# Performance work log

Measured on AMD Instinct MI355X. Metric: run time of the kernel, lower is better.

## Reference

```python
import jax, jax.numpy as jnp
import numpy as np

B, L, D = 32, 128, 128


def setup_inputs() -> dict:
    key = jax.random.key(0)
    ks = jax.random.split(key, 10)
    s = 1.0 / np.sqrt(D)  # torch nn.Linear default init bound
    inp = {
        "input_real": jax.random.normal(ks[0], (B, L, D), jnp.float32),
        "input_imag": jax.random.normal(ks[1], (B, L, D), jnp.float32),
        "Wr1": jax.random.uniform(ks[2], (D, D), jnp.float32, -s, s),
        "br1": jax.random.uniform(ks[3], (D,), jnp.float32, -s, s),
        "Wi1": jax.random.uniform(ks[4], (D, D), jnp.float32, -s, s),
        "bi1": jax.random.uniform(ks[5], (D,), jnp.float32, -s, s),
        "Wr2": jax.random.uniform(ks[6], (D, D), jnp.float32, -s, s),
        "br2": jax.random.uniform(ks[7], (D,), jnp.float32, -s, s),
        "Wi2": jax.random.uniform(ks[8], (D, D), jnp.float32, -s, s),
        "bi2": jax.random.uniform(ks[9], (D,), jnp.float32, -s, s),
    }
    return inp


def reference(input_real, input_imag, Wr1, br1, Wi1, bi1, Wr2, br2, Wi2, bi2):
    # torch Linear: y = x @ W.T + b
    r1 = input_real @ Wr1.T + br1            # (B, L, D)
    i1 = input_imag @ Wi1.T + bi1
    diag_real1 = r1 * r1 - i1 * i1           # Re((r1+i*i1)^2)
    diag_imag1 = 2.0 * r1 * i1               # Im((r1+i*i1)^2)

    r2 = input_real @ Wr2.T + br2
    i2 = input_imag @ Wi2.T + bi2
    diag_real2 = r2 * r2 - i2 * i2
    diag_imag2 = 2.0 * r2 * i2

    # attention over sequence positions L
    att_real = jax.nn.softmax(jnp.sum(diag_real1 * diag_real2, axis=-1), axis=-1)  # (B, L)
    att_imag = jax.nn.softmax(jnp.sum(diag_imag1 * diag_imag2, axis=-1), axis=-1)  # (B, L)

    # Weighted sum over L of per-token complex outer products, without
    # materializing the (B, L, D, D) intermediates the torch code builds:
    # Matrix_real[l] = r2 r2^T - i2 i2^T ; Matrix_imag[l] = i2 r2^T + r2 i2^T
    Mr = (jnp.einsum('bl,bld,ble->bde', att_real, r2, r2)
          - jnp.einsum('bl,bld,ble->bde', att_real, i2, i2))   # (B, D, D)
    Mi = (jnp.einsum('bl,bld,ble->bde', att_imag, i2, r2)
          + jnp.einsum('bl,bld,ble->bde', att_imag, r2, i2))   # (B, D, D)
    return (Mr, Mi)
```

## Files before the change

### kernel.cpp

```cpp
#include <hip/hip_runtime.h>
#include <hip/hip_bf16.h>
#include <math.h>

#define NB 32
#define NL 128
#define ND 128

typedef __attribute__((ext_vector_type(8))) short bf16x8;
typedef __attribute__((ext_vector_type(4))) float f32x4;

union F4  { float4 v; float f[4]; };
union BF8 { bf16x8 v; ushort u[8]; };

__device__ inline ushort f2bf(float f) {
    __hip_bfloat16 h = __float2bfloat16(f);
    union { __hip_bfloat16 h; ushort u; } c; c.h = h; return c.u;
}
__device__ inline float bf2f(ushort u) {
    union { unsigned int i; float f; } c; c.i = ((unsigned int)u) << 16; return c.f;
}
__device__ inline short2 bsplit(float f) {
    ushort hu = f2bf(f);
    short2 r;
    r.x = (short)hu;
    r.y = (short)f2bf(f - bf2f(hu));
    return r;
}

__global__ __launch_bounds__(256) void k_proj(
    const float* __restrict__ xr, const float* __restrict__ xi,
    const float* __restrict__ Wr1, const float* __restrict__ br1,
    const float* __restrict__ Wi1, const float* __restrict__ bi1,
    const float* __restrict__ Wr2, const float* __restrict__ br2,
    const float* __restrict__ Wi2, const float* __restrict__ bi2,
    ushort* __restrict__ gtb, float* __restrict__ lgG)
{
    __shared__ float lgpart[2 * 4 * 16];

    const int bid   = blockIdx.x;
    const int t     = threadIdx.x;
    const int w     = t >> 6;
    const int lane  = t & 63;
    const int l15   = lane & 15;
    const int koff8 = (lane >> 4) * 8;
    const int b     = bid >> 3;
    const int lt    = bid & 7;
    const int arowg = b * NL + lt * 16 + l15;

    bf16x8 axh[2][4], axl[2][4];
    {
        const float* xs[2] = {xr, xi};
#pragma unroll
        for (int arr = 0; arr < 2; ++arr)
#pragma unroll
            for (int ks = 0; ks < 4; ++ks) {
                const float* p = xs[arr] + (size_t)arowg * ND + ks * 32 + koff8;
                F4 f0, f1;
                f0.v = *(const float4*)&p[0];
                f1.v = *(const float4*)&p[4];
                bf16x8 h, l;
#pragma unroll
                for (int e = 0; e < 4; ++e) {
                    short2 s = bsplit(f0.f[e]); h[e] = s.x; l[e] = s.y;
                }
#pragma unroll
                for (int e = 0; e < 4; ++e) {
                    short2 s = bsplit(f1.f[e]); h[4 + e] = s.x; l[4 + e] = s.y;
                }
                axh[arr][ks] = h;
                axl[arr][ks] = l;
            }
    }

    f32x4 acc[4][2];
#pragma unroll
    for (int m = 0; m < 4; ++m)
#pragma unroll
        for (int n = 0; n < 2; ++n) acc[m][n] = (f32x4){0.f, 0.f, 0.f, 0.f};

    {
        const float* Ws[4] = {Wr1, Wi1, Wr2, Wi2};
#pragma unroll
        for (int mat = 0; mat < 4; ++mat) {
            const int arr = mat & 1;
#pragma unroll
            for (int n = 0; n < 2; ++n) {
                const float* wrow = Ws[mat] + (size_t)((w * 2 + n) * 16 + l15) * ND;
#pragma unroll
                for (int ks = 0; ks < 4; ++ks) {
                    F4 f0, f1;
                    f0.v = *(const float4*)&wrow[ks * 32 + koff8];
                    f1.v = *(const float4*)&wrow[ks * 32 + koff8 + 4];
                    bf16x8 bh, bl;
#pragma unroll
                    for (int e = 0; e < 4; ++e) {
                        short2 s = bsplit(f0.f[e]); bh[e] = s.x; bl[e] = s.y;
                    }
#pragma unroll
                    for (int e = 0; e < 4; ++e) {
                        short2 s = bsplit(f1.f[e]); bh[4 + e] = s.x; bl[4 + e] = s.y;
                    }
                    acc[mat][n] = __builtin_amdgcn_mfma_f32_16x16x32_bf16(axh[arr][ks], bh, acc[mat][n], 0, 0, 0);
                    acc[mat][n] = __builtin_amdgcn_mfma_f32_16x16x32_bf16(axh[arr][ks], bl, acc[mat][n], 0, 0, 0);
                    acc[mat][n] = __builtin_amdgcn_mfma_f32_16x16x32_bf16(axl[arr][ks], bh, acc[mat][n], 0, 0, 0);
                }
            }
        }
    }

    float pR[4] = {0.f, 0.f, 0.f, 0.f};
    float pI[4] = {0.f, 0.f, 0.f, 0.f};
    const int lbase = lt * 16 + (lane >> 4) * 4;
#pragma unroll
    for (int n = 0; n < 2; ++n) {
        const int d = (w * 2 + n) * 16 + l15;
        const float b0 = br1[d], b1 = bi1[d], b2 = br2[d], b3 = bi2[d];
        ushort g2[4], g3[4];
#pragma unroll
        for (int r = 0; r < 4; ++r) {
            float y0 = acc[0][n][r] + b0;
            float y1 = acc[1][n][r] + b1;
            float y2 = acc[2][n][r] + b2;
            float y3 = acc[3][n][r] + b3;
            pR[r] += (y0 * y0 - y1 * y1) * (y2 * y2 - y3 * y3);
            pI[r] += 4.f * y0 * y1 * y2 * y3;
            g2[r] = f2bf(y2);
            g3[r] = f2bf(y3);
        }
        ushort4 q2 = {g2[0], g2[1], g2[2], g2[3]};
        ushort4 q3 = {g3[0], g3[1], g3[2], g3[3]};
        *(ushort4*)&gtb[((size_t)(0 * NB + b) * ND + d) * NL + lbase] = q2;
        *(ushort4*)&gtb[((size_t)(1 * NB + b) * ND + d) * NL + lbase] = q3;
    }

#pragma unroll
    for (int off = 1; off < 16; off <<= 1)
#pragma unroll
        for (int r = 0; r < 4; ++r) {
            pR[r] += __shfl_xor(pR[r], off);
            pI[r] += __shfl_xor(pI[r], off);
        }
    if (l15 == 0) {
        const int row = (lane >> 4) * 4;
#pragma unroll
        for (int r = 0; r < 4; ++r) {
            lgpart[(0 * 4 + w) * 16 + row + r] = pR[r];
            lgpart[(1 * 4 + w) * 16 + row + r] = pI[r];
        }
    }
    __syncthreads();
    if (t < 32) {
        const int c = t >> 4, row = t & 15;
        float s = lgpart[(c * 4 + 0) * 16 + row] + lgpart[(c * 4 + 1) * 16 + row]
                + lgpart[(c * 4 + 2) * 16 + row] + lgpart[(c * 4 + 3) * 16 + row];
        lgG[(size_t)(c * NB + b) * NL + lt * 16 + row] = s;
    }
}

__global__ __launch_bounds__(256) void k_gram(
    const ushort* __restrict__ gtb, const float* __restrict__ lgG,
    float* __restrict__ out)
{
    extern __shared__ char L[];
    float* wfl  = (float*)(L + 65536);
    float* wred = (float*)(L + 66048);

    const int bid   = blockIdx.x;
    const int t     = threadIdx.x;
    const int w     = t >> 6;
    const int lane  = t & 63;
    const int l15   = lane & 15;
    const int koff8 = (lane >> 4) * 8;
    const int koffb = koff8 * 2;

    const int b    = bid >> 3;
    const int sub  = bid & 7;
    const int term = sub >> 2;
    const int dq   = (sub >> 1) & 1;
    const int eo   = sub & 1;

    float sv = 0.f, se = 0.f;
    if (t < 128) {
        sv = lgG[(size_t)(term * NB + b) * NL + t];
        float m = sv;
#pragma unroll
        for (int off = 1; off < 64; off <<= 1) m = fmaxf(m, __shfl_xor(m, off));
        if (lane == 0) wred[w] = m;
    }
    __syncthreads();
    if (t < 128) {
        float m = fmaxf(wred[0], wred[1]);
        se = expf(sv - m);
        float s = se;
#pragma unroll
        for (int off = 1; off < 64; off <<= 1) s += __shfl_xor(s, off);
        if (lane == 0) wred[2 + w] = s;
    }
    __syncthreads();
    if (t < 128) wfl[t] = se / (wred[2] + wred[3]);

#pragma unroll
    for (int j = 0; j < 16; ++j) {
        int u    = t + 256 * j;
        int arr  = u >> 11;
        int row  = (u >> 4) & 127;
        int slot = u & 15;
        bf16x8 v = *(const bf16x8*)&gtb[((size_t)(arr * NB + b) * ND + row) * NL + slot * 8];
        *(bf16x8*)(L + arr * 32768 + row * 256 + ((slot * 16) ^ ((row & 7) << 4))) = v;
    }
    __syncthreads();

    f32x4 accP[4], accN[4];
#pragma unroll
    for (int nt = 0; nt < 4; ++nt) {
        accP[nt] = (f32x4){0.f, 0.f, 0.f, 0.f};
        accN[nt] = (f32x4){0.f, 0.f, 0.f, 0.f};
    }

#pragma unroll
    for (int ks = 0; ks < 4; ++ks) {
        F4 w0, w1;
        w0.v = *(const float4*)&wfl[ks * 32 + koff8];
        w1.v = *(const float4*)&wfl[ks * 32 + koff8 + 4];
        float wv[8] = {w0.f[0], w0.f[1], w0.f[2], w0.f[3],
                       w1.f[0], w1.f[1], w1.f[2], w1.f[3]};

        const int ar = dq * 64 + w * 16 + l15;
        const int ab = ar * 256 + (((ks * 64) + koffb) ^ ((ar & 7) << 4));
        BF8 a0; a0.v = *(const bf16x8*)(L + ab);
        BF8 a1; a1.v = *(const bf16x8*)(L + 32768 + ab);
        bf16x8 s0, s1;
#pragma unroll
        for (int e = 0; e < 8; ++e) {
            s0[e] = (short)f2bf(bf2f(a0.u[e]) * wv[e]);
            s1[e] = (short)f2bf(bf2f(a1.u[e]) * wv[e]);
        }
        bf16x8 aP = term ? s1 : s0;
        bf16x8 aN = term ? s0 : s1;

#pragma unroll
        for (int nt = 0; nt < 4; ++nt) {
            const int br = eo * 64 + nt * 16 + l15;
            const int bb = br * 256 + (((ks * 64) + koffb) ^ ((br & 7) << 4));
            bf16x8 b0 = *(const bf16x8*)(L + bb);
            bf16x8 b1 = *(const bf16x8*)(L + 32768 + bb);
            accP[nt] = __builtin_amdgcn_mfma_f32_16x16x32_bf16(aP, b0, accP[nt], 0, 0, 0);
            accN[nt] = __builtin_amdgcn_mfma_f32_16x16x32_bf16(aN, b1, accN[nt], 0, 0, 0);
        }
    }

    const float sgn = term ? 1.f : -1.f;
    float* dst = out + (size_t)term * NB * ND * ND + (size_t)b * ND * ND;
    const int rb = dq * 64 + w * 16 + (lane >> 4) * 4;
#pragma unroll
    for (int nt = 0; nt < 4; ++nt) {
        const int ec = eo * 64 + nt * 16 + l15;
#pragma unroll
        for (int r = 0; r < 4; ++r)
            dst[(size_t)(rb + r) * ND + ec] = accP[nt][r] + sgn * accN[nt][r];
    }
}

extern "C" void kernel_launch(void* const* d_in, const int* in_sizes, int n_in,
                              void* d_out, int out_size, void* d_ws, size_t ws_size,
                              hipStream_t stream)
{
    const float* xr  = (const float*)d_in[0];
    const float* xi  = (const float*)d_in[1];
    const float* Wr1 = (const float*)d_in[2];
    const float* br1 = (const float*)d_in[3];
    const float* Wi1 = (const float*)d_in[4];
    const float* bi1 = (const float*)d_in[5];
    const float* Wr2 = (const float*)d_in[6];
    const float* br2 = (const float*)d_in[7];
    const float* Wi2 = (const float*)d_in[8];
    const float* bi2 = (const float*)d_in[9];

    ushort* gtb = (ushort*)d_ws;
    float*  lgG = (float*)(gtb + 2 * NB * ND * NL);

    (void)hipFuncSetAttribute((const void*)k_gram,
                              hipFuncAttributeMaxDynamicSharedMemorySize, 66560);

    hipLaunchKernelGGL(k_proj, dim3(256), dim3(256), 0, stream,
                       xr, xi, Wr1, br1, Wi1, bi1, Wr2, br2, Wi2, bi2,
                       gtb, lgG);
    hipLaunchKernelGGL(k_gram, dim3(256), dim3(256), 66560, stream,
                       gtb, lgG, (float*)d_out);
}
```

Measured before the change: 25.25 us.

## Fuse projection and gram kernels into one launch with per-batch atomic counters

Merges the two kernels into a single 512-block launch. The first 256 blocks compute the projections and bump a per-batch counter after a threadfence, and the remaining blocks spin on that counter before doing softmax and the gram MFMAs. This removes the kernel-to-kernel launch gap and lets gram work for early batches overlap projection for later ones. It adds a memset launch, spin-wait overhead, and a deadlock risk if consumer blocks take all the slots before producers are scheduled. The projection blocks also now request 66 KB of dynamic LDS, which may lower their occupancy.

```diff
diff --git a/kernel.cpp b/kernel.cpp
--- a/kernel.cpp
+++ b/kernel.cpp
@@ -27,143 +27,16 @@
     return r;
 }
 
-__global__ __launch_bounds__(256) void k_proj(
+__global__ __launch_bounds__(256) void k_all(
     const float* __restrict__ xr, const float* __restrict__ xi,
     const float* __restrict__ Wr1, const float* __restrict__ br1,
     const float* __restrict__ Wi1, const float* __restrict__ bi1,
     const float* __restrict__ Wr2, const float* __restrict__ br2,
     const float* __restrict__ Wi2, const float* __restrict__ bi2,
-    ushort* __restrict__ gtb, float* __restrict__ lgG)
-{
-    __shared__ float lgpart[2 * 4 * 16];
-
-    const int bid   = blockIdx.x;
-    const int t     = threadIdx.x;
-    const int w     = t >> 6;
-    const int lane  = t & 63;
-    const int l15   = lane & 15;
-    const int koff8 = (lane >> 4) * 8;
-    const int b     = bid >> 3;
-    const int lt    = bid & 7;
-    const int arowg = b * NL + lt * 16 + l15;
-
-    bf16x8 axh[2][4], axl[2][4];
-    {
-        const float* xs[2] = {xr, xi};
-#pragma unroll
-        for (int arr = 0; arr < 2; ++arr)
-#pragma unroll
-            for (int ks = 0; ks < 4; ++ks) {
-                const float* p = xs[arr] + (size_t)arowg * ND + ks * 32 + koff8;
-                F4 f0, f1;
-                f0.v = *(const float4*)&p[0];
-                f1.v = *(const float4*)&p[4];
-                bf16x8 h, l;
-#pragma unroll
-                for (int e = 0; e < 4; ++e) {
-                    short2 s = bsplit(f0.f[e]); h[e] = s.x; l[e] = s.y;
-                }
-#pragma unroll
-                for (int e = 0; e < 4; ++e) {
-                    short2 s = bsplit(f1.f[e]); h[4 + e] = s.x; l[4 + e] = s.y;
-                }
-                axh[arr][ks] = h;
-                axl[arr][ks] = l;
-            }
-    }
-
-    f32x4 acc[4][2];
-#pragma unroll
-    for (int m = 0; m < 4; ++m)
-#pragma unroll
-        for (int n = 0; n < 2; ++n) acc[m][n] = (f32x4){0.f, 0.f, 0.f, 0.f};
-
-    {
-        const float* Ws[4] = {Wr1, Wi1, Wr2, Wi2};
-#pragma unroll
-        for (int mat = 0; mat < 4; ++mat) {
-            const int arr = mat & 1;
-#pragma unroll
-            for (int n = 0; n < 2; ++n) {
-                const float* wrow = Ws[mat] + (size_t)((w * 2 + n) * 16 + l15) * ND;
-#pragma unroll
-                for (int ks = 0; ks < 4; ++ks) {
-                    F4 f0, f1;
-                    f0.v = *(const float4*)&wrow[ks * 32 + koff8];
-                    f1.v = *(const float4*)&wrow[ks * 32 + koff8 + 4];
-                    bf16x8 bh, bl;
-#pragma unroll
-                    for (int e = 0; e < 4; ++e) {
-                        short2 s = bsplit(f0.f[e]); bh[e] = s.x; bl[e] = s.y;
-                    }
-#pragma unroll
-                    for (int e = 0; e < 4; ++e) {
-                        short2 s = bsplit(f1.f[e]); bh[4 + e] = s.x; bl[4 + e] = s.y;
-                    }
-                    acc[mat][n] = __builtin_amdgcn_mfma_f32_16x16x32_bf16(axh[arr][ks], bh, acc[mat][n], 0, 0, 0);
-                    acc[mat][n] = __builtin_amdgcn_mfma_f32_16x16x32_bf16(axh[arr][ks], bl, acc[mat][n], 0, 0, 0);
-                    acc[mat][n] = __builtin_amdgcn_mfma_f32_16x16x32_bf16(axl[arr][ks], bh, acc[mat][n], 0, 0, 0);
-                }
-            }
-        }
-    }
-
-    float pR[4] = {0.f, 0.f, 0.f, 0.f};
-    float pI[4] = {0.f, 0.f, 0.f, 0.f};
-    const int lbase = lt * 16 + (lane >> 4) * 4;
-#pragma unroll
-    for (int n = 0; n < 2; ++n) {
-        const int d = (w * 2 + n) * 16 + l15;
-        const float b0 = br1[d], b1 = bi1[d], b2 = br2[d], b3 = bi2[d];
-        ushort g2[4], g3[4];
-#pragma unroll
-        for (int r = 0; r < 4; ++r) {
-            float y0 = acc[0][n][r] + b0;
-            float y1 = acc[1][n][r] + b1;
-            float y2 = acc[2][n][r] + b2;
-            float y3 = acc[3][n][r] + b3;
-            pR[r] += (y0 * y0 - y1 * y1) * (y2 * y2 - y3 * y3);
-            pI[r] += 4.f * y0 * y1 * y2 * y3;
-            g2[r] = f2bf(y2);
-            g3[r] = f2bf(y3);
-        }
-        ushort4 q2 = {g2[0], g2[1], g2[2], g2[3]};
-        ushort4 q3 = {g3[0], g3[1], g3[2], g3[3]};
-        *(ushort4*)&gtb[((size_t)(0 * NB + b) * ND + d) * NL + lbase] = q2;
-        *(ushort4*)&gtb[((size_t)(1 * NB + b) * ND + d) * NL + lbase] = q3;
-    }
-
-#pragma unroll
-    for (int off = 1; off < 16; off <<= 1)
-#pragma unroll
-        for (int r = 0; r < 4; ++r) {
-            pR[r] += __shfl_xor(pR[r], off);
-            pI[r] += __shfl_xor(pI[r], off);
-        }
-    if (l15 == 0) {
-        const int row = (lane >> 4) * 4;
-#pragma unroll
-        for (int r = 0; r < 4; ++r) {
-            lgpart[(0 * 4 + w) * 16 + row + r] = pR[r];
-            lgpart[(1 * 4 + w) * 16 + row + r] = pI[r];
-        }
-    }
-    __syncthreads();
-    if (t < 32) {
-        const int c = t >> 4, row = t & 15;
-        float s = lgpart[(c * 4 + 0) * 16 + row] + lgpart[(c * 4 + 1) * 16 + row]
-                + lgpart[(c * 4 + 2) * 16 + row] + lgpart[(c * 4 + 3) * 16 + row];
-        lgG[(size_t)(c * NB + b) * NL + lt * 16 + row] = s;
-    }
-}
-
-__global__ __launch_bounds__(256) void k_gram(
-    const ushort* __restrict__ gtb, const float* __restrict__ lgG,
+    int* __restrict__ cnt, ushort* __restrict__ gtb, float* __restrict__ lgG,
     float* __restrict__ out)
 {
     extern __shared__ char L[];
-    float* wfl  = (float*)(L + 65536);
-    float* wred = (float*)(L + 66048);
 
     const int bid   = blockIdx.x;
     const int t     = threadIdx.x;
@@ -173,91 +46,224 @@
     const int koff8 = (lane >> 4) * 8;
     const int koffb = koff8 * 2;
 
-    const int b    = bid >> 3;
-    const int sub  = bid & 7;
-    const int term = sub >> 2;
-    const int dq   = (sub >> 1) & 1;
-    const int eo   = sub & 1;
-
-    float sv = 0.f, se = 0.f;
-    if (t < 128) {
-        sv = lgG[(size_t)(term * NB + b) * NL + t];
-        float m = sv;
-#pragma unroll
-        for (int off = 1; off < 64; off <<= 1) m = fmaxf(m, __shfl_xor(m, off));
-        if (lane == 0) wred[w] = m;
-    }
-    __syncthreads();
-    if (t < 128) {
-        float m = fmaxf(wred[0], wred[1]);
-        se = expf(sv - m);
-        float s = se;
-#pragma unroll
-        for (int off = 1; off < 64; off <<= 1) s += __shfl_xor(s, off);
-        if (lane == 0) wred[2 + w] = s;
-    }
-    __syncthreads();
-    if (t < 128) wfl[t] = se / (wred[2] + wred[3]);
-
-#pragma unroll
-    for (int j = 0; j < 16; ++j) {
-        int u    = t + 256 * j;
-        int arr  = u >> 11;
-        int row  = (u >> 4) & 127;
-        int slot = u & 15;
-        bf16x8 v = *(const bf16x8*)&gtb[((size_t)(arr * NB + b) * ND + row) * NL + slot * 8];
-        *(bf16x8*)(L + arr * 32768 + row * 256 + ((slot * 16) ^ ((row & 7) << 4))) = v;
-    }
-    __syncthreads();
-
-    f32x4 accP[4], accN[4];
-#pragma unroll
-    for (int nt = 0; nt < 4; ++nt) {
-        accP[nt] = (f32x4){0.f, 0.f, 0.f, 0.f};
-        accN[nt] = (f32x4){0.f, 0.f, 0.f, 0.f};
-    }
-
-#pragma unroll
-    for (int ks = 0; ks < 4; ++ks) {
-        F4 w0, w1;
-        w0.v = *(const float4*)&wfl[ks * 32 + koff8];
-        w1.v = *(const float4*)&wfl[ks * 32 + koff8 + 4];
-        float wv[8] = {w0.f[0], w0.f[1], w0.f[2], w0.f[3],
-                       w1.f[0], w1.f[1], w1.f[2], w1.f[3]};
-
-        const int ar = dq * 64 + w * 16 + l15;
-        const int ab = ar * 256 + (((ks * 64) + koffb) ^ ((ar & 7) << 4));
-        BF8 a0; a0.v = *(const bf16x8*)(L + ab);
-        BF8 a1; a1.v = *(const bf16x8*)(L + 32768 + ab);
-        bf16x8 s0, s1;
-#pragma unroll
-        for (int e = 0; e < 8; ++e) {
-            s0[e] = (short)f2bf(bf2f(a0.u[e]) * wv[e]);
-            s1[e] = (short)f2bf(bf2f(a1.u[e]) * wv[e]);
-        }
-        bf16x8 aP = term ? s1 : s0;
-        bf16x8 aN = term ? s0 : s1;
-
+    if (bid < 256) {
+        float* lgpart = (float*)L;
+        const int b     = bid >> 3;
+        const int lt    = bid & 7;
+        const int arowg = b * NL + lt * 16 + l15;
+
+        bf16x8 axh[2][4], axl[2][4];
+        {
+            const float* xs[2] = {xr, xi};
+#pragma unroll
+            for (int arr = 0; arr < 2; ++arr)
+#pragma unroll
+                for (int ks = 0; ks < 4; ++ks) {
+                    const float* p = xs[arr] + (size_t)arowg * ND + ks * 32 + koff8;
+                    F4 f0, f1;
+                    f0.v = *(const float4*)&p[0];
+                    f1.v = *(const float4*)&p[4];
+                    bf16x8 h, l;
+#pragma unroll
+                    for (int e = 0; e < 4; ++e) {
+                        short2 s = bsplit(f0.f[e]); h[e] = s.x; l[e] = s.y;
+                    }
+#pragma unroll
+                    for (int e = 0; e < 4; ++e) {
+                        short2 s = bsplit(f1.f[e]); h[4 + e] = s.x; l[4 + e] = s.y;
+                    }
+                    axh[arr][ks] = h;
+                    axl[arr][ks] = l;
+                }
+        }
+
+        f32x4 acc[4][2];
+#pragma unroll
+        for (int m = 0; m < 4; ++m)
+#pragma unroll
+            for (int n = 0; n < 2; ++n) acc[m][n] = (f32x4){0.f, 0.f, 0.f, 0.f};
+
+        {
+            const float* Ws[4] = {Wr1, Wi1, Wr2, Wi2};
+#pragma unroll
+            for (int mat = 0; mat < 4; ++mat) {
+                const int arr = mat & 1;
+#pragma unroll
+                for (int n = 0; n < 2; ++n) {
+                    const float* wrow = Ws[mat] + (size_t)((w * 2 + n) * 16 + l15) * ND;
+#pragma unroll
+                    for (int ks = 0; ks < 4; ++ks) {
+                        F4 f0, f1;
+                        f0.v = *(const float4*)&wrow[ks * 32 + koff8];
+                        f1.v = *(const float4*)&wrow[ks * 32 + koff8 + 4];
+                        bf16x8 bh, bl;
+#pragma unroll
+                        for (int e = 0; e < 4; ++e) {
+                            short2 s = bsplit(f0.f[e]); bh[e] = s.x; bl[e] = s.y;
+                        }
+#pragma unroll
+                        for (int e = 0; e < 4; ++e) {
+                            short2 s = bsplit(f1.f[e]); bh[4 + e] = s.x; bl[4 + e] = s.y;
+                        }
+                        acc[mat][n] = __builtin_amdgcn_mfma_f32_16x16x32_bf16(axh[arr][ks], bh, acc[mat][n], 0, 0, 0);
+                        acc[mat][n] = __builtin_amdgcn_mfma_f32_16x16x32_bf16(axh[arr][ks], bl, acc[mat][n], 0, 0, 0);
+                        acc[mat][n] = __builtin_amdgcn_mfma_f32_16x16x32_bf16(axl[arr][ks], bh, acc[mat][n], 0, 0, 0);
+                    }
+                }
+            }
+        }
+
+        float pR[4] = {0.f, 0.f, 0.f, 0.f};
+        float pI[4] = {0.f, 0.f, 0.f, 0.f};
+        const int lbase = lt * 16 + (lane >> 4) * 4;
+#pragma unroll
+        for (int n = 0; n < 2; ++n) {
+            const int d = (w * 2 + n) * 16 + l15;
+            const float b0 = br1[d], b1 = bi1[d], b2 = br2[d], b3 = bi2[d];
+            ushort g2[4], g3[4];
+#pragma unroll
+            for (int r = 0; r < 4; ++r) {
+                float y0 = acc[0][n][r] + b0;
+                float y1 = acc[1][n][r] + b1;
+                float y2 = acc[2][n][r] + b2;
+                float y3 = acc[3][n][r] + b3;
+                pR[r] += (y0 * y0 - y1 * y1) * (y2 * y2 - y3 * y3);
+                pI[r] += 4.f * y0 * y1 * y2 * y3;
+                g2[r] = f2bf(y2);
+                g3[r] = f2bf(y3);
+            }
+            ushort4 q2 = {g2[0], g2[1], g2[2], g2[3]};
+            ushort4 q3 = {g3[0], g3[1], g3[2], g3[3]};
+            *(ushort4*)&gtb[((size_t)(0 * NB + b) * ND + d) * NL + lbase] = q2;
+            *(ushort4*)&gtb[((size_t)(1 * NB + b) * ND + d) * NL + lbase] = q3;
+        }
+
+#pragma unroll
+        for (int off = 1; off < 16; off <<= 1)
+#pragma unroll
+            for (int r = 0; r < 4; ++r) {
+                pR[r] += __shfl_xor(pR[r], off);
+                pI[r] += __shfl_xor(pI[r], off);
+            }
+        if (l15 == 0) {
+            const int row = (lane >> 4) * 4;
+#pragma unroll
+            for (int r = 0; r < 4; ++r) {
+                lgpart[(0 * 4 + w) * 16 + row + r] = pR[r];
+                lgpart[(1 * 4 + w) * 16 + row + r] = pI[r];
+            }
+        }
+        __syncthreads();
+        if (t < 32) {
+            const int c = t >> 4, row = t & 15;
+            float s = lgpart[(c * 4 + 0) * 16 + row] + lgpart[(c * 4 + 1) * 16 + row]
+                    + lgpart[(c * 4 + 2) * 16 + row] + lgpart[(c * 4 + 3) * 16 + row];
+            lgG[(size_t)(c * NB + b) * NL + lt * 16 + row] = s;
+        }
+
+        __threadfence();
+        __syncthreads();
+        if (t == 0) atomicAdd(&cnt[b * 16], 1);
+    } else {
+        float* wfl  = (float*)(L + 65536);
+        float* wred = (float*)(L + 66048);
+
+        const int gb   = bid - 256;
+        const int b    = gb >> 3;
+        const int sub  = gb & 7;
+        const int term = sub >> 2;
+        const int dq   = (sub >> 1) & 1;
+        const int eo   = sub & 1;
+
+        if (t == 0) {
+            while (__hip_atomic_load(&cnt[b * 16], __ATOMIC_ACQUIRE,
+                                     __HIP_MEMORY_SCOPE_AGENT) < 8) {
+                __builtin_amdgcn_s_sleep(8);
+            }
+        }
+        __syncthreads();
+        __threadfence();
+
+        float sv = 0.f, se = 0.f;
+        if (t < 128) {
+            sv = lgG[(size_t)(term * NB + b) * NL + t];
+            float m = sv;
+#pragma unroll
+            for (int off = 1; off < 64; off <<= 1) m = fmaxf(m, __shfl_xor(m, off));
+            if (lane == 0) wred[w] = m;
+        }
+        __syncthreads();
+        if (t < 128) {
+            float m = fmaxf(wred[0], wred[1]);
+            se = expf(sv - m);
+            float s = se;
+#pragma unroll
+            for (int off = 1; off < 64; off <<= 1) s += __shfl_xor(s, off);
+            if (lane == 0) wred[2 + w] = s;
+        }
+        __syncthreads();
+        if (t < 128) wfl[t] = se / (wred[2] + wred[3]);
+
+#pragma unroll
+        for (int j = 0; j < 16; ++j) {
+            int u    = t + 256 * j;
+            int arr  = u >> 11;
+            int row  = (u >> 4) & 127;
+            int slot = u & 15;
+            bf16x8 v = *(const bf16x8*)&gtb[((size_t)(arr * NB + b) * ND + row) * NL + slot * 8];
+            *(bf16x8*)(L + arr * 32768 + row * 256 + ((slot * 16) ^ ((row & 7) << 4))) = v;
+        }
+        __syncthreads();
+
+        f32x4 accP[4], accN[4];
 #pragma unroll
         for (int nt = 0; nt < 4; ++nt) {
-            const int br = eo * 64 + nt * 16 + l15;
-            const int bb = br * 256 + (((ks * 64) + koffb) ^ ((br & 7) << 4));
-            bf16x8 b0 = *(const bf16x8*)(L + bb);
-            bf16x8 b1 = *(const bf16x8*)(L + 32768 + bb);
-            accP[nt] = __builtin_amdgcn_mfma_f32_16x16x32_bf16(aP, b0, accP[nt], 0, 0, 0);
-            accN[nt] = __builtin_amdgcn_mfma_f32_16x16x32_bf16(aN, b1, accN[nt], 0, 0, 0);
-        }
-    }
-
-    const float sgn = term ? 1.f : -1.f;
-    float* dst = out + (size_t)term * NB * ND * ND + (size_t)b * ND * ND;
-    const int rb = dq * 64 + w * 16 + (lane >> 4) * 4;
-#pragma unroll
-    for (int nt = 0; nt < 4; ++nt) {
-        const int ec = eo * 64 + nt * 16 + l15;
-#pragma unroll
-        for (int r = 0; r < 4; ++r)
-            dst[(size_t)(rb + r) * ND + ec] = accP[nt][r] + sgn * accN[nt][r];
+            accP[nt] = (f32x4){0.f, 0.f, 0.f, 0.f};
+            accN[nt] = (f32x4){0.f, 0.f, 0.f, 0.f};
+        }
+
+#pragma unroll
+        for (int ks = 0; ks < 4; ++ks) {
+            F4 w0, w1;
+            w0.v = *(const float4*)&wfl[ks * 32 + koff8];
+            w1.v = *(const float4*)&wfl[ks * 32 + koff8 + 4];
+            float wv[8] = {w0.f[0], w0.f[1], w0.f[2], w0.f[3],
+                           w1.f[0], w1.f[1], w1.f[2], w1.f[3]};
+
+            const int ar = dq * 64 + w * 16 + l15;
+            const int ab = ar * 256 + (((ks * 64) + koffb) ^ ((ar & 7) << 4));
+            BF8 a0; a0.v = *(const bf16x8*)(L + ab);
+            BF8 a1; a1.v = *(const bf16x8*)(L + 32768 + ab);
+            bf16x8 s0, s1;
+#pragma unroll
+            for (int e = 0; e < 8; ++e) {
+                s0[e] = (short)f2bf(bf2f(a0.u[e]) * wv[e]);
+                s1[e] = (short)f2bf(bf2f(a1.u[e]) * wv[e]);
+            }
+            bf16x8 aP = term ? s1 : s0;
+            bf16x8 aN = term ? s0 : s1;
+
+#pragma unroll
+            for (int nt = 0; nt < 4; ++nt) {
+                const int br = eo * 64 + nt * 16 + l15;
+                const int bb = br * 256 + (((ks * 64) + koffb) ^ ((br & 7) << 4));
+                bf16x8 b0 = *(const bf16x8*)(L + bb);
+                bf16x8 b1 = *(const bf16x8*)(L + 32768 + bb);
+                accP[nt] = __builtin_amdgcn_mfma_f32_16x16x32_bf16(aP, b0, accP[nt], 0, 0, 0);
+                accN[nt] = __builtin_amdgcn_mfma_f32_16x16x32_bf16(aN, b1, accN[nt], 0, 0, 0);
+            }
+        }
+
+        const float sgn = term ? 1.f : -1.f;
+        float* dst = out + (size_t)term * NB * ND * ND + (size_t)b * ND * ND;
+        const int rb = dq * 64 + w * 16 + (lane >> 4) * 4;
+#pragma unroll
+        for (int nt = 0; nt < 4; ++nt) {
+            const int ec = eo * 64 + nt * 16 + l15;
+#pragma unroll
+            for (int r = 0; r < 4; ++r)
+                dst[(size_t)(rb + r) * ND + ec] = accP[nt][r] + sgn * accN[nt][r];
+        }
     }
 }
 
@@ -276,15 +282,15 @@
     const float* Wi2 = (const float*)d_in[8];
     const float* bi2 = (const float*)d_in[9];
 
-    ushort* gtb = (ushort*)d_ws;
+    int*    cnt = (int*)d_ws;
+    ushort* gtb = (ushort*)((char*)d_ws + 2048);
     float*  lgG = (float*)(gtb + 2 * NB * ND * NL);
 
-    (void)hipFuncSetAttribute((const void*)k_gram,
+    (void)hipFuncSetAttribute((const void*)k_all,
                               hipFuncAttributeMaxDynamicSharedMemorySize, 66560);
 
-    hipLaunchKernelGGL(k_proj, dim3(256), dim3(256), 0, stream,
+    hipMemsetAsync(cnt, 0, 2048, stream);
+    hipLaunchKernelGGL(k_all, dim3(512), dim3(256), 66560, stream,
                        xr, xi, Wr1, br1, Wi1, bi1, Wr2, br2, Wi2, bi2,
-                       gtb, lgG);
-    hipLaunchKernelGGL(k_gram, dim3(256), dim3(256), 66560, stream,
-                       gtb, lgG, (float*)d_out);
-}
+                       cnt, gtb, lgG, (float*)d_out);
+}
```

Result: slower. 98.93 us (+291.8%).

## Fuse projection and gram kernels, recomputing projections per block in LDS

Applied to the files above, without the earlier changes.

Merges the projection and gram kernels into one launch. Each block recomputes the full per-batch projections and writes the bf16 r2/i2 tiles directly into swizzled shared memory, and computes the attention logits locally. This removes the intermediate global buffer round trip and the second launch. The cost is 8x redundant projection MFMA and conversion work across the blocks of each batch.

```diff
diff --git a/kernel.cpp b/kernel.cpp
--- a/kernel.cpp
+++ b/kernel.cpp
@@ -27,145 +27,19 @@
     return r;
 }
 
-__global__ __launch_bounds__(256) void k_proj(
+__global__ __launch_bounds__(256, 1) void k_one(
     const float* __restrict__ xr, const float* __restrict__ xi,
     const float* __restrict__ Wr1, const float* __restrict__ br1,
     const float* __restrict__ Wi1, const float* __restrict__ bi1,
     const float* __restrict__ Wr2, const float* __restrict__ br2,
     const float* __restrict__ Wi2, const float* __restrict__ bi2,
-    ushort* __restrict__ gtb, float* __restrict__ lgG)
-{
-    __shared__ float lgpart[2 * 4 * 16];
-
-    const int bid   = blockIdx.x;
-    const int t     = threadIdx.x;
-    const int w     = t >> 6;
-    const int lane  = t & 63;
-    const int l15   = lane & 15;
-    const int koff8 = (lane >> 4) * 8;
-    const int b     = bid >> 3;
-    const int lt    = bid & 7;
-    const int arowg = b * NL + lt * 16 + l15;
-
-    bf16x8 axh[2][4], axl[2][4];
-    {
-        const float* xs[2] = {xr, xi};
-#pragma unroll
-        for (int arr = 0; arr < 2; ++arr)
-#pragma unroll
-            for (int ks = 0; ks < 4; ++ks) {
-                const float* p = xs[arr] + (size_t)arowg * ND + ks * 32 + koff8;
-                F4 f0, f1;
-                f0.v = *(const float4*)&p[0];
-                f1.v = *(const float4*)&p[4];
-                bf16x8 h, l;
-#pragma unroll
-                for (int e = 0; e < 4; ++e) {
-                    short2 s = bsplit(f0.f[e]); h[e] = s.x; l[e] = s.y;
-                }
-#pragma unroll
-                for (int e = 0; e < 4; ++e) {
-                    short2 s = bsplit(f1.f[e]); h[4 + e] = s.x; l[4 + e] = s.y;
-                }
-                axh[arr][ks] = h;
-                axl[arr][ks] = l;
-            }
-    }
-
-    f32x4 acc[4][2];
-#pragma unroll
-    for (int m = 0; m < 4; ++m)
-#pragma unroll
-        for (int n = 0; n < 2; ++n) acc[m][n] = (f32x4){0.f, 0.f, 0.f, 0.f};
-
-    {
-        const float* Ws[4] = {Wr1, Wi1, Wr2, Wi2};
-#pragma unroll
-        for (int mat = 0; mat < 4; ++mat) {
-            const int arr = mat & 1;
-#pragma unroll
-            for (int n = 0; n < 2; ++n) {
-                const float* wrow = Ws[mat] + (size_t)((w * 2 + n) * 16 + l15) * ND;
-#pragma unroll
-                for (int ks = 0; ks < 4; ++ks) {
-                    F4 f0, f1;
-                    f0.v = *(const float4*)&wrow[ks * 32 + koff8];
-                    f1.v = *(const float4*)&wrow[ks * 32 + koff8 + 4];
-                    bf16x8 bh, bl;
-#pragma unroll
-                    for (int e = 0; e < 4; ++e) {
-                        short2 s = bsplit(f0.f[e]); bh[e] = s.x; bl[e] = s.y;
-                    }
-#pragma unroll
-                    for (int e = 0; e < 4; ++e) {
-                        short2 s = bsplit(f1.f[e]); bh[4 + e] = s.x; bl[4 + e] = s.y;
-                    }
-                    acc[mat][n] = __builtin_amdgcn_mfma_f32_16x16x32_bf16(axh[arr][ks], bh, acc[mat][n], 0, 0, 0);
-                    acc[mat][n] = __builtin_amdgcn_mfma_f32_16x16x32_bf16(axh[arr][ks], bl, acc[mat][n], 0, 0, 0);
-                    acc[mat][n] = __builtin_amdgcn_mfma_f32_16x16x32_bf16(axl[arr][ks], bh, acc[mat][n], 0, 0, 0);
-                }
-            }
-        }
-    }
-
-    float pR[4] = {0.f, 0.f, 0.f, 0.f};
-    float pI[4] = {0.f, 0.f, 0.f, 0.f};
-    const int lbase = lt * 16 + (lane >> 4) * 4;
-#pragma unroll
-    for (int n = 0; n < 2; ++n) {
-        const int d = (w * 2 + n) * 16 + l15;
-        const float b0 = br1[d], b1 = bi1[d], b2 = br2[d], b3 = bi2[d];
-        ushort g2[4], g3[4];
-#pragma unroll
-        for (int r = 0; r < 4; ++r) {
-            float y0 = acc[0][n][r] + b0;
-            float y1 = acc[1][n][r] + b1;
-            float y2 = acc[2][n][r] + b2;
-            float y3 = acc[3][n][r] + b3;
-            pR[r] += (y0 * y0 - y1 * y1) * (y2 * y2 - y3 * y3);
-            pI[r] += 4.f * y0 * y1 * y2 * y3;
-            g2[r] = f2bf(y2);
-            g3[r] = f2bf(y3);
-        }
-        ushort4 q2 = {g2[0], g2[1], g2[2], g2[3]};
-        ushort4 q3 = {g3[0], g3[1], g3[2], g3[3]};
-        *(ushort4*)&gtb[((size_t)(0 * NB + b) * ND + d) * NL + lbase] = q2;
-        *(ushort4*)&gtb[((size_t)(1 * NB + b) * ND + d) * NL + lbase] = q3;
-    }
-
-#pragma unroll
-    for (int off = 1; off < 16; off <<= 1)
-#pragma unroll
-        for (int r = 0; r < 4; ++r) {
-            pR[r] += __shfl_xor(pR[r], off);
-            pI[r] += __shfl_xor(pI[r], off);
-        }
-    if (l15 == 0) {
-        const int row = (lane >> 4) * 4;
-#pragma unroll
-        for (int r = 0; r < 4; ++r) {
-            lgpart[(0 * 4 + w) * 16 + row + r] = pR[r];
-            lgpart[(1 * 4 + w) * 16 + row + r] = pI[r];
-        }
-    }
-    __syncthreads();
-    if (t < 32) {
-        const int c = t >> 4, row = t & 15;
-        float s = lgpart[(c * 4 + 0) * 16 + row] + lgpart[(c * 4 + 1) * 16 + row]
-                + lgpart[(c * 4 + 2) * 16 + row] + lgpart[(c * 4 + 3) * 16 + row];
-        lgG[(size_t)(c * NB + b) * NL + lt * 16 + row] = s;
-    }
-}
-
-__global__ __launch_bounds__(256) void k_gram(
-    const ushort* __restrict__ gtb, const float* __restrict__ lgG,
     float* __restrict__ out)
 {
     extern __shared__ char L[];
-    float* wfl  = (float*)(L + 65536);
-    float* wred = (float*)(L + 66048);
-
-    const int bid   = blockIdx.x;
+    float* lgs  = (float*)(L + 65536);
+    float* wfl  = (float*)(L + 66560);
+    float* wred = (float*)(L + 67072);
+
     const int t     = threadIdx.x;
     const int w     = t >> 6;
     const int lane  = t & 63;
@@ -173,15 +47,133 @@
     const int koff8 = (lane >> 4) * 8;
     const int koffb = koff8 * 2;
 
+    const int bid  = blockIdx.x;
     const int b    = bid >> 3;
     const int sub  = bid & 7;
     const int term = sub >> 2;
     const int dq   = (sub >> 1) & 1;
     const int eo   = sub & 1;
 
+    bf16x8 axh[2][2][4], axl[2][2][4];
+    {
+        const float* xs[2] = {xr, xi};
+#pragma unroll
+        for (int lt2 = 0; lt2 < 2; ++lt2) {
+            const int arowg = b * NL + (w + 4 * lt2) * 16 + l15;
+#pragma unroll
+            for (int arr = 0; arr < 2; ++arr)
+#pragma unroll
+                for (int ks = 0; ks < 4; ++ks) {
+                    const float* p = xs[arr] + (size_t)arowg * ND + ks * 32 + koff8;
+                    F4 f0, f1;
+                    f0.v = *(const float4*)&p[0];
+                    f1.v = *(const float4*)&p[4];
+                    bf16x8 h, l;
+#pragma unroll
+                    for (int e = 0; e < 4; ++e) {
+                        short2 s = bsplit(f0.f[e]); h[e] = s.x; l[e] = s.y;
+                    }
+#pragma unroll
+                    for (int e = 0; e < 4; ++e) {
+                        short2 s = bsplit(f1.f[e]); h[4 + e] = s.x; l[4 + e] = s.y;
+                    }
+                    axh[lt2][arr][ks] = h;
+                    axl[lt2][arr][ks] = l;
+                }
+        }
+    }
+
+    float pR[2][4] = {{0.f,0.f,0.f,0.f},{0.f,0.f,0.f,0.f}};
+    float pI[2][4] = {{0.f,0.f,0.f,0.f},{0.f,0.f,0.f,0.f}};
+    {
+        const float* Ws[4] = {Wr1, Wi1, Wr2, Wi2};
+#pragma unroll
+        for (int nt = 0; nt < 8; ++nt) {
+            f32x4 acc[4][2];
+#pragma unroll
+            for (int m = 0; m < 4; ++m)
+#pragma unroll
+                for (int lt2 = 0; lt2 < 2; ++lt2)
+                    acc[m][lt2] = (f32x4){0.f, 0.f, 0.f, 0.f};
+
+#pragma unroll
+            for (int mat = 0; mat < 4; ++mat) {
+                const int arr = mat & 1;
+                const float* wrow = Ws[mat] + (size_t)(nt * 16 + l15) * ND;
+#pragma unroll
+                for (int ks = 0; ks < 4; ++ks) {
+                    F4 f0, f1;
+                    f0.v = *(const float4*)&wrow[ks * 32 + koff8];
+                    f1.v = *(const float4*)&wrow[ks * 32 + koff8 + 4];
+                    bf16x8 bh, bl;
+#pragma unroll
+                    for (int e = 0; e < 4; ++e) {
+                        short2 s = bsplit(f0.f[e]); bh[e] = s.x; bl[e] = s.y;
+                    }
+#pragma unroll
+                    for (int e = 0; e < 4; ++e) {
+                        short2 s = bsplit(f1.f[e]); bh[4 + e] = s.x; bl[4 + e] = s.y;
+                    }
+                    acc[mat][0] = __builtin_amdgcn_mfma_f32_16x16x32_bf16(axh[0][arr][ks], bh, acc[mat][0], 0, 0, 0);
+                    acc[mat][0] = __builtin_amdgcn_mfma_f32_16x16x32_bf16(axh[0][arr][ks], bl, acc[mat][0], 0, 0, 0);
+                    acc[mat][0] = __builtin_amdgcn_mfma_f32_16x16x32_bf16(axl[0][arr][ks], bh, acc[mat][0], 0, 0, 0);
+                    acc[mat][1] = __builtin_amdgcn_mfma_f32_16x16x32_bf16(axh[1][arr][ks], bh, acc[mat][1], 0, 0, 0);
+                    acc[mat][1] = __builtin_amdgcn_mfma_f32_16x16x32_bf16(axh[1][arr][ks], bl, acc[mat][1], 0, 0, 0);
+                    acc[mat][1] = __builtin_amdgcn_mfma_f32_16x16x32_bf16(axl[1][arr][ks], bh, acc[mat][1], 0, 0, 0);
+                }
+            }
+
+            const int d  = nt * 16 + l15;
+            const float b0 = br1[d], b1 = bi1[d], b2 = br2[d], b3 = bi2[d];
+#pragma unroll
+            for (int lt2 = 0; lt2 < 2; ++lt2) {
+                const int lb = (w + 4 * lt2) * 16 + (lane >> 4) * 4;
+                ushort g2[4], g3[4];
+#pragma unroll
+                for (int r = 0; r < 4; ++r) {
+                    float y0 = acc[0][lt2][r] + b0;
+                    float y1 = acc[1][lt2][r] + b1;
+                    float y2 = acc[2][lt2][r] + b2;
+                    float y3 = acc[3][lt2][r] + b3;
+                    pR[lt2][r] += (y0 * y0 - y1 * y1) * (y2 * y2 - y3 * y3);
+                    pI[lt2][r] += 4.f * y0 * y1 * y2 * y3;
+                    g2[r] = f2bf(y2);
+                    g3[r] = f2bf(y3);
+                }
+                const int byte0 = d * 256 + ((lb * 2) ^ ((d & 7) << 4));
+                *(unsigned int*)(L + byte0)             = (unsigned int)g2[0] | ((unsigned int)g2[1] << 16);
+                *(unsigned int*)(L + byte0 + 4)         = (unsigned int)g2[2] | ((unsigned int)g2[3] << 16);
+                *(unsigned int*)(L + 32768 + byte0)     = (unsigned int)g3[0] | ((unsigned int)g3[1] << 16);
+                *(unsigned int*)(L + 32768 + byte0 + 4) = (unsigned int)g3[2] | ((unsigned int)g3[3] << 16);
+            }
+        }
+    }
+
+#pragma unroll
+    for (int off = 1; off < 16; off <<= 1)
+#pragma unroll
+        for (int lt2 = 0; lt2 < 2; ++lt2)
+#pragma unroll
+            for (int r = 0; r < 4; ++r) {
+                pR[lt2][r] += __shfl_xor(pR[lt2][r], off);
+                pI[lt2][r] += __shfl_xor(pI[lt2][r], off);
+            }
+    if (l15 == 0) {
+#pragma unroll
+        for (int lt2 = 0; lt2 < 2; ++lt2) {
+            const int row = (w + 4 * lt2) * 16 + (lane >> 4) * 4;
+#pragma unroll
+            for (int r = 0; r < 4; ++r) {
+                lgs[row + r]       = pR[lt2][r];
+                lgs[128 + row + r] = pI[lt2][r];
+            }
+        }
+    }
+    __syncthreads();
+
     float sv = 0.f, se = 0.f;
     if (t < 128) {
-        sv = lgG[(size_t)(term * NB + b) * NL + t];
+        sv = lgs[term * 128 + t];
         float m = sv;
 #pragma unroll
         for (int off = 1; off < 64; off <<= 1) m = fmaxf(m, __shfl_xor(m, off));
@@ -198,16 +190,6 @@
     }
     __syncthreads();
     if (t < 128) wfl[t] = se / (wred[2] + wred[3]);
-
-#pragma unroll
-    for (int j = 0; j < 16; ++j) {
-        int u    = t + 256 * j;
-        int arr  = u >> 11;
-        int row  = (u >> 4) & 127;
-        int slot = u & 15;
-        bf16x8 v = *(const bf16x8*)&gtb[((size_t)(arr * NB + b) * ND + row) * NL + slot * 8];
-        *(bf16x8*)(L + arr * 32768 + row * 256 + ((slot * 16) ^ ((row & 7) << 4))) = v;
-    }
     __syncthreads();
 
     f32x4 accP[4], accN[4];
@@ -276,15 +258,10 @@
     const float* Wi2 = (const float*)d_in[8];
     const float* bi2 = (const float*)d_in[9];
 
-    ushort* gtb = (ushort*)d_ws;
-    float*  lgG = (float*)(gtb + 2 * NB * ND * NL);
-
-    (void)hipFuncSetAttribute((const void*)k_gram,
-                              hipFuncAttributeMaxDynamicSharedMemorySize, 66560);
-
-    hipLaunchKernelGGL(k_proj, dim3(256), dim3(256), 0, stream,
+    (void)hipFuncSetAttribute((const void*)k_one,
+                              hipFuncAttributeMaxDynamicSharedMemorySize, 67584);
+
+    hipLaunchKernelGGL(k_one, dim3(256), dim3(256), 67584, stream,
                        xr, xi, Wr1, br1, Wi1, bi1, Wr2, br2, Wi2, bi2,
-                       gtb, lgG);
-    hipLaunchKernelGGL(k_gram, dim3(256), dim3(256), 66560, stream,
-                       gtb, lgG, (float*)d_out);
-}
+                       (float*)d_out);
+}
```

New measurement: 70.50 us. 2.79x slower.
